# Kernel tuning notes

Measured on AMD Instinct MI355X. Metric: run time of the kernel, lower is better.

The kernel has to match this reference:

```python
import jax, jax.numpy as jnp
import numpy as np

N_E = 1024      # codes per sub-codebook
E_DIM = 64      # code dimension
BETA = 0.25     # commitment cost (VectorQuantizer(n_e, e_dim, 0.25))


def setup_inputs() -> dict:
    key = jax.random.key(0)
    k1, k2 = jax.random.split(key)
    bs, c, h, w = 16, 512, 32, 32
    m = c // E_DIM  # 8 sub-codebooks
    z = jax.random.normal(k1, (bs, c, h, w), dtype=jnp.float32)
    # taming-style init: uniform(-1/n_e, 1/n_e)
    codebooks = jax.random.uniform(
        k2, (m, N_E, E_DIM), dtype=jnp.float32,
        minval=-1.0 / N_E, maxval=1.0 / N_E)
    return {"z": z, "codebooks": codebooks}


def reference(z, codebooks):
    bs, c, h, w = z.shape
    m, n_e, e_dim = codebooks.shape
    N = bs * h * w
    # [bs,c,h,w] -> [bs,h,w,c] -> [m, N, e_dim]: batched over all m sub-codebooks at once
    zf = z.transpose(0, 2, 3, 1).reshape(N, m, e_dim).transpose(1, 0, 2)

    # squared L2 distances: ||z||^2 + ||e||^2 - 2 z.e   -> [m, N, n_e]
    d = ((zf ** 2).sum(-1, keepdims=True)
         + (codebooks ** 2).sum(-1)[:, None, :]
         - 2.0 * jnp.einsum('mnd,mkd->mnk', zf, codebooks))
    idx = jnp.argmin(d, axis=-1)  # [m, N]

    # gather nearest codes: [m, N, e_dim]
    zq = jnp.take_along_axis(codebooks, idx[:, :, None], axis=1)

    # per-sub-codebook VQ loss, summed over m (loss = sum(loss_list))
    codebook_loss = jnp.mean((jax.lax.stop_gradient(zq) - zf) ** 2, axis=(1, 2))
    commit_loss = jnp.mean((zq - jax.lax.stop_gradient(zf)) ** 2, axis=(1, 2))
    loss = jnp.sum(codebook_loss + BETA * commit_loss)

    # straight-through estimator
    zq_st = zf + jax.lax.stop_gradient(zq - zf)

    # reassemble: [m,N,d] -> [N,m*d] -> [bs,h,w,c] -> [bs,c,h,w]
    z_vq = zq_st.transpose(1, 0, 2).reshape(bs, h, w, c).transpose(0, 3, 1, 2)

    # concat of per-codebook index tensors along dim 0
    min_encoding_indices = idx.reshape(-1)  # [m*N]
    # per-code occupancy counts summed over the m codebooks -> [n_e]
    bin_count = jnp.zeros((n_e,), jnp.int32).at[min_encoding_indices].add(1)

    return z_vq, loss, min_encoding_indices, bin_count
```

## Files before the change

### kernel.cpp

```cpp
#include <hip/hip_runtime.h>
#include <cfloat>

#define BS 16
#define CC 512
#define HWD 1024
#define NN 16384
#define MM 8
#define NE 1024
#define ED 64

#define LOSS_OFF 8388608
#define IDX_OFF  8388609
#define BIN_OFF  8519681

#define TAU 4e-5f
#define UWIN 400u

#define WS_B     0
#define WS_IDX   32768
#define WS_CNT   557056
#define WS_LIST  557088
#define WS_OF    688160
#define WS_CAND  720928
#define WS_BMAT  3866656

typedef __attribute__((ext_vector_type(8))) short bf16x8;
typedef __attribute__((ext_vector_type(16))) float f32x16;

__device__ __forceinline__ unsigned short f2bf(float f) {
    unsigned int u = __float_as_uint(f);
    unsigned int r = (u + 0x7fffu + ((u >> 16) & 1u)) >> 16;
    return (unsigned short)r;
}
__device__ __forceinline__ float bf2f(unsigned short h) {
    return __uint_as_float(((unsigned int)h) << 16);
}
__device__ __forceinline__ unsigned umin_(unsigned a, unsigned b) { return a < b ? a : b; }
__device__ __forceinline__ unsigned umax_(unsigned a, unsigned b) { return a > b ? a : b; }
__device__ __forceinline__ unsigned umin3(unsigned a, unsigned b, unsigned c) {
    return umin_(umin_(a, b), c);
}

__device__ __forceinline__ float mul_rn(float a, float b) {
#pragma clang fp contract(off)
    return a * b;
}
__device__ __forceinline__ float add_rn(float a, float b) {
#pragma clang fp contract(off)
    return a + b;
}
__device__ __forceinline__ float sub_rn(float a, float b) {
#pragma clang fp contract(off)
    return a - b;
}

__device__ __forceinline__ float np_sumsq64(const float* x) {
    float r[8];
#pragma unroll
    for (int j = 0; j < 8; ++j) r[j] = mul_rn(x[j], x[j]);
#pragma unroll
    for (int i = 8; i < 64; i += 8) {
#pragma unroll
        for (int j = 0; j < 8; ++j) r[j] = add_rn(r[j], mul_rn(x[i + j], x[i + j]));
    }
    return add_rn(add_rn(add_rn(r[0], r[1]), add_rn(r[2], r[3])),
                  add_rn(add_rn(r[4], r[5]), add_rn(r[6], r[7])));
}

__device__ __forceinline__ float np_dot64(const float* zsh, const float4* cr4) {
    float v0 = 0.f, v1 = 0.f, v2 = 0.f, v3 = 0.f;
#pragma unroll
    for (int t = 0; t < 4; ++t) {
        float4 e0 = cr4[t * 4 + 0];
        float4 e1 = cr4[t * 4 + 1];
        float4 e2 = cr4[t * 4 + 2];
        float4 e3 = cr4[t * 4 + 3];
        const int d0 = 16 * t;
        v0 = add_rn(mul_rn(zsh[d0 + 0], e0.x),
             add_rn(mul_rn(zsh[d0 + 4], e1.x),
             add_rn(mul_rn(zsh[d0 + 8], e2.x),
             add_rn(mul_rn(zsh[d0 + 12], e3.x), v0))));
        v1 = add_rn(mul_rn(zsh[d0 + 1], e0.y),
             add_rn(mul_rn(zsh[d0 + 5], e1.y),
             add_rn(mul_rn(zsh[d0 + 9], e2.y),
             add_rn(mul_rn(zsh[d0 + 13], e3.y), v1))));
        v2 = add_rn(mul_rn(zsh[d0 + 2], e0.z),
             add_rn(mul_rn(zsh[d0 + 6], e1.z),
             add_rn(mul_rn(zsh[d0 + 10], e2.z),
             add_rn(mul_rn(zsh[d0 + 14], e3.z), v2))));
        v3 = add_rn(mul_rn(zsh[d0 + 3], e0.w),
             add_rn(mul_rn(zsh[d0 + 7], e1.w),
             add_rn(mul_rn(zsh[d0 + 11], e2.w),
             add_rn(mul_rn(zsh[d0 + 15], e3.w), v3))));
    }
    return add_rn(add_rn(v0, v1), add_rn(v2, v3));
}

__global__ __launch_bounds__(256) void prep_kernel(const float* __restrict__ cb,
                                                   float* __restrict__ Bhat,
                                                   uint4* __restrict__ Bmat,
                                                   float* __restrict__ out,
                                                   int* __restrict__ cnt) {
    const int tid = threadIdx.x;
    if (blockIdx.x < 32) {
        int i = blockIdx.x * 256 + tid;
        if (i == 0) { out[LOSS_OFF] = 0.0f; cnt[0] = 0; cnt[1] = 0; }
        if (i < NE) out[BIN_OFF + i] = 0.0f;
        const float4* r4 = (const float4*)(cb + (size_t)i * ED);
        float x[ED];
#pragma unroll
        for (int q = 0; q < 16; ++q) {
            float4 v = r4[q];
            x[q*4+0] = v.x; x[q*4+1] = v.y; x[q*4+2] = v.z; x[q*4+3] = v.w;
        }
        Bhat[i] = np_sumsq64(x);
        return;
    }
    int t = (blockIdx.x - 32) * 256 + tid;
    int lane = t & 63;
    int ct = (t >> 6) & 31;
    int rem = t >> 11;
    int c = rem % 13;
    int m = rem / 13;
    int h = lane >> 5;
    int k = ct * 32 + (lane & 31);

    unsigned short v[8];
#pragma unroll
    for (int j = 0; j < 8; ++j) v[j] = 0;

    if (c < 12) {
        int d0 = 16 * (c & 3) + 8 * h;
        const float* e = cb + ((size_t)m * NE + k) * ED + d0;
#pragma unroll
        for (int j = 0; j < 8; ++j) {
            float f = -2.0f * e[j];
            unsigned short hi = f2bf(f);
            v[j] = (c >= 4 && c < 8) ? f2bf(f - bf2f(hi)) : hi;
        }
    } else if (h == 0) {
        const float* e = cb + ((size_t)m * NE + k) * ED;
        float s = 0.f;
#pragma unroll
        for (int d = 0; d < ED; ++d) s += e[d] * e[d];
        v[0] = f2bf(s);
        v[1] = 0x3F80;
    }
    uint4 o;
    o.x = (unsigned)v[0] | ((unsigned)v[1] << 16);
    o.y = (unsigned)v[2] | ((unsigned)v[3] << 16);
    o.z = (unsigned)v[4] | ((unsigned)v[5] << 16);
    o.w = (unsigned)v[6] | ((unsigned)v[7] << 16);
    Bmat[t] = o;
}

__global__ __launch_bounds__(512, 4) void argmin_kernel(
        const float* __restrict__ z, const uint4* __restrict__ Bmat,
        int* __restrict__ idx_out, int* __restrict__ cnt,
        int* __restrict__ list, unsigned short* __restrict__ cand) {
    const int tid = threadIdx.x;
    const int m = blockIdx.y;
    const int row0 = blockIdx.x * 256;
    const int w = tid >> 6;
    const int l = tid & 63;
    const int h = l >> 5;
    const int r5 = l & 31;

    __shared__ uint4 ldsB[2][13 * 2 * 64];

    const int n_mine = row0 + w * 32 + r5;
    const int b = n_mine >> 10;
    const int hw = n_mine & (HWD - 1);
    const float* zbase = z + (((size_t)(b * CC + m * ED)) << 10) + hw;

    bf16x8 zh[4], zl[4];
#pragma unroll
    for (int i = 0; i < 4; ++i) {
        int o = 2 * i + h;
#pragma unroll
        for (int j = 0; j < 8; ++j) {
            float f = zbase[(size_t)(8 * o + j) << 10];
            unsigned short hb = f2bf(f);
            unsigned short lb = f2bf(f - bf2f(hb));
            zh[i][j] = (short)hb;
            zl[i][j] = (short)lb;
        }
    }
    bf16x8 ones12 = {0, 0, 0, 0, 0, 0, 0, 0};
    if (h == 0) { ones12[0] = (short)0x3F80; ones12[1] = (short)0x3F80; }

    unsigned rbm = 0xFFFFFFF0u, rsec = 0xFFFFFFFFu, rinfo = 0;
    int ccnt = 0;
    unsigned short* myslots = cand + ((size_t)(m * NN + n_mine) * 2 + h) * 6;

    auto stage = [&](int g, int bufi) {
        for (int seg = w; seg < 26; seg += 8) {
            int c = seg >> 1, ct2 = seg & 1;
            const uint4* src = Bmat +
                ((size_t)((m * 13 + c) * 32 + (g * 2 + ct2)) << 6) + l;
            uint4* dst = &ldsB[bufi][(c * 2 + ct2) * 64];
            __builtin_amdgcn_global_load_lds(
                (const __attribute__((address_space(1))) unsigned int*)src,
                (__attribute__((address_space(3))) unsigned int*)dst, 16, 0, 0);
        }
    };

    stage(0, 0);
    __syncthreads();
    int buf = 0;
    for (int g = 0; g < 16; ++g) {
        if (g < 15) stage(g + 1, buf ^ 1);

#pragma unroll
        for (int ctl = 0; ctl < 2; ++ctl) {
            f32x16 acc;
#pragma unroll
            for (int s = 0; s < 16; ++s) acc[s] = 0.0f;
#pragma unroll
            for (int c = 0; c < 13; ++c) {
                bf16x8 af = *(const bf16x8*)&ldsB[buf][(c * 2 + ctl) * 64 + l];
                bf16x8 bfr = (c < 8) ? zh[c & 3] : ((c < 12) ? zl[c & 3] : ones12);
                acc = __builtin_amdgcn_mfma_f32_32x32x16_bf16(af, bfr, acc, 0, 0, 0);
            }
            unsigned u[16];
#pragma unroll
            for (int s = 0; s < 16; ++s)
                u[s] = (__float_as_uint(acc[s]) & 0xFFFFFFF0u) | (unsigned)s;
            unsigned b0 = umin_(u[0], u[1]),  s0 = umax_(u[0], u[1]);
            unsigned b1 = umin_(u[2], u[3]),  s1 = umax_(u[2], u[3]);
            unsigned b2 = umin_(u[4], u[5]),  s2 = umax_(u[4], u[5]);
            unsigned b3 = umin_(u[6], u[7]),  s3 = umax_(u[6], u[7]);
            unsigned b4 = umin_(u[8], u[9]),  s4 = umax_(u[8], u[9]);
            unsigned b5 = umin_(u[10], u[11]), s5 = umax_(u[10], u[11]);
            unsigned b6 = umin_(u[12], u[13]), s6 = umax_(u[12], u[13]);
            unsigned b7 = umin_(u[14], u[15]), s7 = umax_(u[14], u[15]);
            unsigned B0 = umin_(b0, b1), S0 = umin3(umax_(b0, b1), s0, s1);
            unsigned B1 = umin_(b2, b3), S1 = umin3(umax_(b2, b3), s2, s3);
            unsigned B2 = umin_(b4, b5), S2 = umin3(umax_(b4, b5), s4, s5);
            unsigned B3 = umin_(b6, b7), S3 = umin3(umax_(b6, b7), s6, s7);
            unsigned C0 = umin_(B0, B1), T0 = umin3(umax_(B0, B1), S0, S1);
            unsigned C1 = umin_(B2, B3), T1 = umin3(umax_(B2, B3), S2, S3);
            unsigned bt = umin_(C0, C1), st = umin3(umax_(C0, C1), T0, T1);

            unsigned tile = (unsigned)(g * 2 + ctl);
            unsigned oldrbm = rbm;
            bool take = bt < oldrbm;
            if (take && bt + UWIN < oldrbm) ccnt = 0;
            unsigned other = take ? oldrbm : bt;
            rsec = umin3(rsec, st, other);
            rbm = take ? bt : oldrbm;
            rinfo = take ? ((tile << 4) | (bt & 15u)) : rinfo;

            unsigned limit = rbm + UWIN;
            if (bt < limit) {
#pragma unroll
                for (int s = 0; s < 16; ++s) {
                    if (u[s] < limit) {
                        if (ccnt < 6)
                            myslots[ccnt] = (unsigned short)(
                                tile * 32u + ((unsigned)s & 3u) +
                                8u * ((unsigned)s >> 2) + 4u * (unsigned)h);
                        ccnt++;
                    }
                }
            }
        }
        __syncthreads();
        buf ^= 1;
    }

    int pcnt = __shfl_xor(ccnt, 32, 64);

    unsigned ss = rinfo & 15u, tile = rinfo >> 4;
    int k = (int)(tile * 32 + (ss & 3u) + 8u * (ss >> 2) + 4u * (unsigned)h);
    unsigned orbm = __shfl_xor(rbm, 32, 64);
    int ok = __shfl_xor(k, 32, 64);
    unsigned orsec = __shfl_xor(rsec, 32, 64);
    bool take = orbm < rbm;
    unsigned lose = take ? rbm : orbm;
    unsigned fb = take ? orbm : rbm;
    int fk = take ? ok : k;
    unsigned fs = umin3(rsec, orsec, lose);
    if (l < 32) {
        int mn = m * NN + n_mine;
        idx_out[mn] = fk;
        float margin = __uint_as_float(fs & 0xFFFFFFF0u) -
                       __uint_as_float(fb & 0xFFFFFFF0u);
        if (margin < TAU) {
            int p = atomicAdd(cnt, 1);
            if (p < 32768) {
                int c0 = ccnt > 6 ? 7 : ccnt;
                int c1 = pcnt > 6 ? 7 : pcnt;
                list[p] = mn | (c0 << 20) | (c1 << 24);
            }
        }
    }
}

__global__ __launch_bounds__(256) void cand_kernel(
        const float* __restrict__ z, const float* __restrict__ cb,
        const float* __restrict__ Bhat, int* __restrict__ cnt,
        const int* __restrict__ list, const unsigned short* __restrict__ cand,
        int* __restrict__ idx_out, int* __restrict__ oflist) {
    const int tid = threadIdx.x;
    const int lane = tid & 63;
    const int wv = tid >> 6;
    const int wid = (blockIdx.x * 256 + tid) >> 6;
    const int nw = gridDim.x * 4;
    const int total = cnt[0] < 32768 ? cnt[0] : 32768;

    __shared__ float zsh[4][ED];

    for (int r = wid; r < total; r += nw) {
        const int e = list[r];
        const int mn = e & 0xFFFFF;
        const int c0 = (e >> 20) & 15;
        const int c1 = (e >> 24) & 15;
        if (c0 == 7 || c1 == 7) {
            if (lane == 0) {
                int q = atomicAdd(cnt + 1, 1);
                if (q < 8192) oflist[q] = mn;
            }
            continue;
        }
        const int m = mn >> 14;
        const int n = mn & (NN - 1);
        const int b = n >> 10;
        const int hw = n & (HWD - 1);

        zsh[wv][lane] = z[(((size_t)(b * CC + m * ED + lane)) << 10) + hw];

        int kj = -1;
        if (lane < c0) kj = cand[(size_t)mn * 12 + lane];
        else if (lane >= 8 && lane < 8 + c1) kj = cand[(size_t)mn * 12 + 6 + (lane - 8)];

        float A = np_sumsq64(&zsh[wv][0]);

        float dref = FLT_MAX;
        if (kj >= 0) {
            const float4* cr4 = (const float4*)(cb + ((size_t)m * NE + kj) * ED);
            float C = np_dot64(&zsh[wv][0], cr4);
            dref = sub_rn(add_rn(A, Bhat[m * NE + kj]), mul_rn(2.0f, C));
        }
        int kk = (kj >= 0) ? kj : NE;
#pragma unroll
        for (int off = 32; off >= 1; off >>= 1) {
            float ov = __shfl_down(dref, off, 64);
            int oi = __shfl_down(kk, off, 64);
            if (ov < dref || (ov == dref && oi < kk)) { dref = ov; kk = oi; }
        }
        if (lane == 0) idx_out[mn] = kk;
    }
}

__global__ __launch_bounds__(256) void emul_kernel(
        const float* __restrict__ z, const float* __restrict__ cb,
        const float* __restrict__ Bhat, const int* __restrict__ cnt,
        const int* __restrict__ oflist, int* __restrict__ idx_out) {
    const int tid = threadIdx.x;
    const int lane = tid & 63;
    const int w = tid >> 6;
    const int total = cnt[1] < 8192 ? cnt[1] : 8192;

    __shared__ float zsh[ED];
    __shared__ float rbest[4];
    __shared__ int ridx[4];

    for (int r = blockIdx.x; r < total; r += gridDim.x) {
        const int mn = oflist[r];
        const int m = mn >> 14;
        const int n = mn & (NN - 1);
        const int b = n >> 10;
        const int hw = n & (HWD - 1);

        __syncthreads();
        if (tid < ED) {
            const float* zbase = z + (((size_t)(b * CC + m * ED)) << 10) + hw;
            zsh[tid] = zbase[(size_t)tid << 10];
        }
        __syncthreads();

        const float A = np_sumsq64(zsh);
        const float* cbm = cb + (size_t)m * NE * ED;
        const float* Bm = Bhat + m * NE;
        float best = FLT_MAX;
        int bidx = NE;
#pragma unroll
        for (int kk = 0; kk < 4; ++kk) {
            const int k = kk * 256 + tid;
            const float4* cr4 = (const float4*)(cbm + (size_t)k * ED);
            float C = np_dot64(zsh, cr4);
            float dk = sub_rn(add_rn(A, Bm[k]), mul_rn(2.0f, C));
            if (dk < best || (dk == best && k < bidx)) { best = dk; bidx = k; }
        }
#pragma unroll
        for (int off = 32; off >= 1; off >>= 1) {
            float ov = __shfl_down(best, off, 64);
            int oi = __shfl_down(bidx, off, 64);
            if (ov < best || (ov == best && oi < bidx)) { best = ov; bidx = oi; }
        }
        if (lane == 0) { rbest[w] = best; ridx[w] = bidx; }
        __syncthreads();
        if (tid == 0) {
            float bb = rbest[0]; int bi = ridx[0];
#pragma unroll
            for (int i = 1; i < 4; ++i) {
                if (rbest[i] < bb || (rbest[i] == bb && ridx[i] < bi)) {
                    bb = rbest[i]; bi = ridx[i];
                }
            }
            idx_out[mn] = bi;
        }
    }
}

__global__ __launch_bounds__(256) void output_kernel(
        const float* __restrict__ z, const float* __restrict__ cb,
        const int* __restrict__ idx_in, float* __restrict__ out) {
    const int tid = threadIdx.x;
    const int n = blockIdx.x * 256 + tid;
    const int m = blockIdx.y;
    const int b = n >> 10;
    const int hw = n & (HWD - 1);
    const int idx = idx_in[m * NN + n];

    out[IDX_OFF + m * NN + n] = (float)idx;

    const float* cr = cb + ((size_t)m * NE + (size_t)idx) * ED;
    const float* zbase = z + (((size_t)(b * CC + m * ED)) << 10) + hw;
    float* ob = out + (((size_t)(b * CC + m * ED)) << 10) + hw;

    double acc = 0.0;
#pragma unroll
    for (int d = 0; d < ED; ++d) {
        float c = cr[d];
        float zv = zbase[(size_t)d << 10];
        ob[(size_t)d << 10] = c;
        float diff = c - zv;
        acc += (double)diff * (double)diff;
    }

    __shared__ int hist[NE];
#pragma unroll
    for (int i = 0; i < 4; ++i) hist[tid + i * 256] = 0;
    __syncthreads();
    atomicAdd(&hist[idx], 1);

#pragma unroll
    for (int off = 32; off >= 1; off >>= 1)
        acc += __shfl_down(acc, off, 64);
    __shared__ double wsum[4];
    if ((tid & 63) == 0) wsum[tid >> 6] = acc;
    __syncthreads();
    if (tid == 0) {
        double t = wsum[0] + wsum[1] + wsum[2] + wsum[3];
        atomicAdd(out + LOSS_OFF, (float)(t * (1.25 / 1048576.0)));
    }
#pragma unroll
    for (int i = 0; i < 4; ++i) {
        int v = hist[tid + i * 256];
        if (v) atomicAdd(out + BIN_OFF + tid + i * 256, (float)v);
    }
}

extern "C" void kernel_launch(void* const* d_in, const int* in_sizes, int n_in,
                              void* d_out, int out_size, void* d_ws, size_t ws_size,
                              hipStream_t stream) {
    const float* z = (const float*)d_in[0];
    const float* cb = (const float*)d_in[1];
    float* out = (float*)d_out;
    char* ws = (char*)d_ws;
    float* Bhat = (float*)(ws + WS_B);
    int* idxw = (int*)(ws + WS_IDX);
    int* cnt = (int*)(ws + WS_CNT);
    int* list = (int*)(ws + WS_LIST);
    int* oflist = (int*)(ws + WS_OF);
    unsigned short* cand = (unsigned short*)(ws + WS_CAND);
    uint4* Bmat = (uint4*)(ws + WS_BMAT);

    prep_kernel<<<dim3(864), dim3(256), 0, stream>>>(cb, Bhat, Bmat, out, cnt);
    argmin_kernel<<<dim3(NN / 256, MM), dim3(512), 0, stream>>>(
        z, Bmat, idxw, cnt, list, cand);
    cand_kernel<<<dim3(256), dim3(256), 0, stream>>>(
        z, cb, Bhat, cnt, list, cand, idxw, oflist);
    emul_kernel<<<dim3(256), dim3(256), 0, stream>>>(
        z, cb, Bhat, cnt, oflist, idxw);
    output_kernel<<<dim3(NN / 256, MM), dim3(256), 0, stream>>>(z, cb, idxw, out);
}
```

Measured before the change: 191.1 us.

## Triple-buffer codebook staging and keep candidate list in registers

```diff
diff --git a/kernel.cpp b/kernel.cpp
--- a/kernel.cpp
+++ b/kernel.cpp
@@ -166,7 +166,7 @@
     const int h = l >> 5;
     const int r5 = l & 31;
 
-    __shared__ uint4 ldsB[2][13 * 2 * 64];
+    __shared__ uint4 ldsB[3][13 * 2 * 64];
 
     const int n_mine = row0 + w * 32 + r5;
     const int b = n_mine >> 10;
@@ -191,7 +191,13 @@
 
     unsigned rbm = 0xFFFFFFF0u, rsec = 0xFFFFFFFFu, rinfo = 0;
     int ccnt = 0;
-    unsigned short* myslots = cand + ((size_t)(m * NN + n_mine) * 2 + h) * 6;
+    unsigned cq0 = 0, cq1 = 0, cq2 = 0;
+    auto push = [&](unsigned id) {
+        cq2 = (cq2 << 16) | (cq1 >> 16);
+        cq1 = (cq1 << 16) | (cq0 >> 16);
+        cq0 = (cq0 << 16) | (id & 0xFFFFu);
+        ccnt++;
+    };
 
     auto stage = [&](int g, int bufi) {
         for (int seg = w; seg < 26; seg += 8) {
@@ -206,10 +212,15 @@
     };
 
     stage(0, 0);
-    __syncthreads();
-    int buf = 0;
+    stage(1, 1);
+    asm volatile("s_waitcnt vmcnt(3)" ::: "memory");
+    __builtin_amdgcn_s_barrier();
+
+    int bR = 0;
     for (int g = 0; g < 16; ++g) {
-        if (g < 15) stage(g + 1, buf ^ 1);
+        int bW = bR + 2; if (bW >= 3) bW -= 3;
+        if (g < 14) stage(g + 2, bW);
+        const uint4* Bb = &ldsB[bR][0];
 
 #pragma unroll
         for (int ctl = 0; ctl < 2; ++ctl) {
@@ -218,7 +229,7 @@
             for (int s = 0; s < 16; ++s) acc[s] = 0.0f;
 #pragma unroll
             for (int c = 0; c < 13; ++c) {
-                bf16x8 af = *(const bf16x8*)&ldsB[buf][(c * 2 + ctl) * 64 + l];
+                bf16x8 af = *(const bf16x8*)&Bb[(c * 2 + ctl) * 64 + l];
                 bf16x8 bfr = (c < 8) ? zh[c & 3] : ((c < 12) ? zl[c & 3] : ones12);
                 acc = __builtin_amdgcn_mfma_f32_32x32x16_bf16(af, bfr, acc, 0, 0, 0);
             }
@@ -245,28 +256,41 @@
             unsigned tile = (unsigned)(g * 2 + ctl);
             unsigned oldrbm = rbm;
             bool take = bt < oldrbm;
-            if (take && bt + UWIN < oldrbm) ccnt = 0;
-            unsigned other = take ? oldrbm : bt;
-            rsec = umin3(rsec, st, other);
-            rbm = take ? bt : oldrbm;
-            rinfo = take ? ((tile << 4) | (bt & 15u)) : rinfo;
-
-            unsigned limit = rbm + UWIN;
-            if (bt < limit) {
+            unsigned newrbm = take ? bt : oldrbm;
+            unsigned limit = newrbm + UWIN;
+            rsec = umin3(rsec, st, take ? oldrbm : bt);
+            int sbt = (int)(bt & 15u);
+            if (take) {
+                if (bt + UWIN < oldrbm) ccnt = 0;
+                push(tile * 32u + ((unsigned)sbt & 3u) +
+                     8u * ((unsigned)sbt >> 2) + 4u * (unsigned)h);
+                rinfo = (tile << 4) | (unsigned)sbt;
+            }
+            rbm = newrbm;
+            unsigned gatev = take ? st : bt;
+            if (gatev < limit) {
 #pragma unroll
                 for (int s = 0; s < 16; ++s) {
-                    if (u[s] < limit) {
-                        if (ccnt < 6)
-                            myslots[ccnt] = (unsigned short)(
-                                tile * 32u + ((unsigned)s & 3u) +
-                                8u * ((unsigned)s >> 2) + 4u * (unsigned)h);
-                        ccnt++;
-                    }
+                    if (u[s] < limit && !(take && s == sbt))
+                        push(tile * 32u + ((unsigned)s & 3u) +
+                             8u * ((unsigned)s >> 2) + 4u * (unsigned)h);
                 }
             }
         }
-        __syncthreads();
-        buf ^= 1;
+
+        if (g < 14) {
+            asm volatile("s_waitcnt vmcnt(3)" ::: "memory");
+        } else if (g == 14) {
+            asm volatile("s_waitcnt vmcnt(0)" ::: "memory");
+        }
+        if (g < 15) __builtin_amdgcn_s_barrier();
+        bR = (bR == 2) ? 0 : bR + 1;
+    }
+
+    unsigned short* myslots = cand + ((size_t)(m * NN + n_mine) * 2 + h) * 6;
+    if (ccnt) {
+        unsigned* cp = (unsigned*)myslots;
+        cp[0] = cq0; cp[1] = cq1; cp[2] = cq2;
     }
 
     int pcnt = __shfl_xor(ccnt, 32, 64);
```

New measurement: 175.5 us. -8.1%, faster.
